# Kernel optimization log

Measured on AMD Instinct MI355X. Metric: run time of the kernel, lower is better.

Reference implementation:

```python
import jax, jax.numpy as jnp
import numpy as np

HIDDEN = 4544
N_HEADS = 71
HEAD_DIM = 64
SEQ = 2048
ROPE_BASE = 10000.0


def _rope_cos_sin(seq_len, dim, base=ROPE_BASE):
    inv_freq = 1.0 / (base ** (jnp.arange(0, dim, 2, dtype=jnp.float32) / dim))
    t = jnp.arange(seq_len, dtype=jnp.float32)
    freqs = jnp.einsum('i,j->ij', t, inv_freq)          # [s, dim/2]
    emb = jnp.concatenate([freqs, freqs], axis=-1)      # [s, dim]
    return jnp.cos(emb), jnp.sin(emb)


def _rotate_half(x):
    x1, x2 = jnp.split(x, 2, axis=-1)
    return jnp.concatenate([-x2, x1], axis=-1)


def _apply_rope(x, cos, sin):
    # x: [..., s, d]; cos/sin: [s, d] broadcast over leading dims
    return x * cos + _rotate_half(x) * sin


def setup_inputs() -> dict:
    key = jax.random.key(0)
    k1, k2, k3 = jax.random.split(key, 3)
    hidden_states = jax.random.normal(k1, (1, 1, SEQ, HIDDEN), dtype=jnp.float32) * 0.02
    qkv_weight = jax.random.normal(k2, ((N_HEADS + 2) * HEAD_DIM, HIDDEN), dtype=jnp.float32) * 0.02
    dense_weight = jax.random.normal(k3, (HIDDEN, HIDDEN), dtype=jnp.float32) * 0.02
    # causal additive mask, same construction as the torch module (triu of -1e5)
    mask = jnp.triu(jnp.full((SEQ, SEQ), -100000.0, dtype=jnp.float32), k=1)[None, None]
    return {
        'hidden_states': hidden_states,
        'qkv_weight': qkv_weight,
        'dense_weight': dense_weight,
        'attention_mask': mask,
    }


def reference(hidden_states, qkv_weight, dense_weight, attention_mask):
    b = hidden_states.shape[0]
    s = hidden_states.shape[2]
    x = hidden_states[:, 0]                                   # [b, s, H]

    # fused QKV projection (no bias): [b, s, (nH+2)*d]
    fused = jnp.einsum('bsh,oh->bso', x, qkv_weight)

    q = fused[..., : N_HEADS * HEAD_DIM]
    q = q.reshape(b, s, N_HEADS, HEAD_DIM).transpose(0, 2, 1, 3)   # [b, nH, s, d]
    k = fused[..., N_HEADS * HEAD_DIM : (N_HEADS + 1) * HEAD_DIM]  # [b, s, d] (single KV head, MQA)
    v = fused[..., (N_HEADS + 1) * HEAD_DIM :]                     # [b, s, d]

    cos, sin = _rope_cos_sin(s, HEAD_DIM)
    q = _apply_rope(q, cos, sin)
    k = _apply_rope(k, cos, sin)

    scale = 1.0 / np.sqrt(HEAD_DIM).astype(np.float32)
    scores = jnp.einsum('bhqd,bkd->bhqk', q, k) * scale            # [b, nH, s, s]
    scores = scores + attention_mask
    attn = jax.nn.softmax(scores, axis=-1)
    out = jnp.einsum('bhqk,bkd->bhqd', attn, v)                    # [b, nH, s, d]

    out = out.transpose(0, 2, 1, 3).reshape(b, s, N_HEADS * HEAD_DIM)  # concat heads
    out = jnp.einsum('bsh,oh->bso', out, dense_weight)             # dense projection
    return out[:, None]                                            # [b, 1, s, H]
```

## Files before the change

### kernel.cpp

```cpp
#include <hip/hip_runtime.h>

#define SEQ     2048
#define HIDDEN  4544
#define NHEAD   71
#define HD      64
#define QKV_OUT 4672

typedef __bf16    bf16;
typedef _Float16  f16;
typedef __bf16    bf16x8 __attribute__((ext_vector_type(8)));
typedef __bf16    bf16x4 __attribute__((ext_vector_type(4)));
typedef _Float16  f16x4  __attribute__((ext_vector_type(4)));
typedef _Float16  f16x8  __attribute__((ext_vector_type(8)));
typedef float     f32x4  __attribute__((ext_vector_type(4)));

__device__ inline void gl2lds16(const void* g, void* ldsbase) {
  __builtin_amdgcn_global_load_lds(
      (const __attribute__((address_space(1))) unsigned int*)g,
      (__attribute__((address_space(3))) unsigned int*)ldsbase,
      16, 0, 0);
}

__global__ void cvt3_k(const float* __restrict__ a, const float* __restrict__ b,
                       const float* __restrict__ c,
                       bf16* __restrict__ oa, bf16* __restrict__ ob, bf16* __restrict__ oc,
                       int na4, int nb4, int nc4) {
  int i = blockIdx.x * blockDim.x + threadIdx.x;
  const float* src; bf16* dst; int idx;
  if (i < na4)             { src = a; dst = oa; idx = i; }
  else if (i < na4 + nb4)  { src = b; dst = ob; idx = i - na4; }
  else if (i < na4 + nb4 + nc4) { src = c; dst = oc; idx = i - na4 - nb4; }
  else return;
  float4 f = ((const float4*)src)[idx];
  bf16x4 o;
  o[0] = (bf16)f.x; o[1] = (bf16)f.y; o[2] = (bf16)f.z; o[3] = (bf16)f.w;
  *(bf16x4*)(dst + (size_t)idx * 4) = o;
}

__global__ __launch_bounds__(256) void gemm_bt_k(const bf16* __restrict__ A,
                                                 const bf16* __restrict__ B,
                                                 float* __restrict__ C,
                                                 int K, int Nmat, int ldc) {
  __shared__ bf16 lA[2][128 * 32];
  __shared__ bf16 lB[2][128 * 32];
  const int t = threadIdx.x;
  const int lane = t & 63, w = t >> 6;

  const int gx = gridDim.x;
  const int nwg = gx * gridDim.y;
  const int orig = blockIdx.y * gx + blockIdx.x;
  const int swz = (orig & 7) * (nwg >> 3) + (orig >> 3);
  const int m0 = (swz % gx) * 128;
  const int n0 = (swz / gx) * 128;

  const int wm = (w >> 1) * 64, wn = (w & 1) * 64;
  const int qi = lane & 15, grp = lane >> 4;

  const int r0 = t >> 2;
  const int c0 = (t & 3) * 8;
  const bf16* gA0 = A + (size_t)(m0 + r0) * K + c0;
  const bf16* gA1 = A + (size_t)(m0 + 64 + r0) * K + c0;
  int bR0 = n0 + r0;      if (bR0 >= Nmat) bR0 = Nmat - 1;
  int bR1 = n0 + 64 + r0; if (bR1 >= Nmat) bR1 = Nmat - 1;
  const bf16* gB0 = B + (size_t)bR0 * K + c0;
  const bf16* gB1 = B + (size_t)bR1 * K + c0;
  bf16* lA00 = &lA[0][0] + w * 512;
  bf16* lA01 = &lA[0][2048] + w * 512;
  bf16* lA10 = &lA[1][0] + w * 512;
  bf16* lA11 = &lA[1][2048] + w * 512;
  bf16* lB00 = &lB[0][0] + w * 512;
  bf16* lB01 = &lB[0][2048] + w * 512;
  bf16* lB10 = &lB[1][0] + w * 512;
  bf16* lB11 = &lB[1][2048] + w * 512;

  f32x4 acc[4][4] = {};
  for (int k0 = 0; k0 < K; k0 += 64) {
    __syncthreads();
    gl2lds16(gA0 + k0,      lA00);
    gl2lds16(gA1 + k0,      lA01);
    gl2lds16(gA0 + k0 + 32, lA10);
    gl2lds16(gA1 + k0 + 32, lA11);
    gl2lds16(gB0 + k0,      lB00);
    gl2lds16(gB1 + k0,      lB01);
    gl2lds16(gB0 + k0 + 32, lB10);
    gl2lds16(gB1 + k0 + 32, lB11);
    __syncthreads();
#pragma unroll
    for (int half = 0; half < 2; ++half) {
      bf16x8 af[4], bfv[4];
#pragma unroll
      for (int i = 0; i < 4; ++i)
        af[i] = *(const bf16x8*)&lA[half][(wm + i * 16 + qi) * 32 + grp * 8];
#pragma unroll
      for (int i = 0; i < 4; ++i)
        bfv[i] = *(const bf16x8*)&lB[half][(wn + i * 16 + qi) * 32 + grp * 8];
#pragma unroll
      for (int i = 0; i < 4; ++i)
#pragma unroll
        for (int j = 0; j < 4; ++j)
          acc[i][j] = __builtin_amdgcn_mfma_f32_16x16x32_bf16(af[i], bfv[j], acc[i][j], 0, 0, 0);
    }
  }

#pragma unroll
  for (int i = 0; i < 4; ++i) {
    const int row = m0 + wm + i * 16 + grp * 4;
#pragma unroll
    for (int j = 0; j < 4; ++j) {
      const int col = n0 + wn + j * 16 + qi;
      if (col < Nmat) {
#pragma unroll
        for (int r = 0; r < 4; ++r)
          C[(size_t)(row + r) * ldc + col] = acc[i][j][r];
      }
    }
  }
}

#define QSCALE 0.18033688f
__global__ __launch_bounds__(256) void ropekv_k(const float* __restrict__ fused,
                                                bf16* __restrict__ Qb,
                                                bf16* __restrict__ Kf,
                                                f16* __restrict__ Vf) {
  const int s = blockIdx.x, t = threadIdx.x;
  __shared__ float cs[64], sn[64];
  if (t < 64) {
    int i = t & 31;
    double invf = pow(10000.0, -(double)i / 32.0);
    double ang = (double)s * invf;
    cs[t] = (float)cos(ang);
    sn[t] = (float)sin(ang);
  }
  __syncthreads();
  const float* row = fused + (size_t)s * QKV_OUT;

  if (t < 64) {
    const int d = t;
    float x = row[NHEAD * 64 + d], xp = row[NHEAD * 64 + (d ^ 32)];
    float rot = (d < 32) ? -xp : xp;
    Kf[(s >> 4) * 1024 + (d >> 5) * 512 + ((d >> 3) & 3) * 128 + (s & 15) * 8 + (d & 7)] =
        (bf16)(x * cs[d] + rot * sn[d]);
  } else if (t < 128) {
    const int d = t - 64;
    Vf[(s >> 4) * 1024 + (d >> 5) * 512 + ((s >> 2) & 3) * 128 + (d & 15) * 8 +
       ((d >> 4) & 1) * 4 + (s & 3)] = (f16)row[(NHEAD + 1) * 64 + d];
  }

  bf16* qrow = Qb + (size_t)s * HIDDEN;
  for (int u = t; u < NHEAD * 8; u += 256) {
    const int head = u >> 3, c4 = (u & 7) * 4;
    const int e = head * 64 + c4;
    float4 lo = *(const float4*)(row + e);
    float4 hi = *(const float4*)(row + e + 32);
    float xl[4] = {lo.x, lo.y, lo.z, lo.w};
    float xh[4] = {hi.x, hi.y, hi.z, hi.w};
    bf16x4 qlo, qhi;
#pragma unroll
    for (int j = 0; j < 4; ++j) {
      const float c = cs[c4 + j], n = sn[c4 + j];
      qlo[j] = (bf16)((xl[j] * c - xh[j] * n) * QSCALE);
      qhi[j] = (bf16)((xh[j] * c + xl[j] * n) * QSCALE);
    }
    *(bf16x4*)(qrow + e) = qlo;
    *(bf16x4*)(qrow + e + 32) = qhi;
  }
}

__global__ __launch_bounds__(64) void attn_k(const bf16* __restrict__ Qb,
                                             const bf16* __restrict__ Kf,
                                             const f16*  __restrict__ Vf,
                                             bf16* __restrict__ Ao) {
  __shared__ float fl[2 * 16 * 68];
  const int h = blockIdx.y;
  const int b32 = gridDim.x - 1 - blockIdx.x;
  const int lane = threadIdx.x;
  const int qi = lane & 15, grp = lane >> 4;
  const int q0 = b32 * 32;
  const int lastT = b32 >> 1;

  bf16x8 qf[2][2];
#pragma unroll
  for (int qq = 0; qq < 2; ++qq) {
    const bf16* qb = Qb + (size_t)(q0 + qq * 16 + qi) * HIDDEN + h * 64 + grp * 8;
    qf[qq][0] = *(const bf16x8*)qb;
    qf[qq][1] = *(const bf16x8*)(qb + 32);
  }

  f32x4 o[2][4] = {};
  float l[2] = {0.f, 0.f};

  for (int kb = 0; kb <= lastT; ++kb) {
    const bf16* kfp = Kf + (size_t)kb * 4096 + lane * 8;
    bf16x8 kf[4][2];
#pragma unroll
    for (int kk = 0; kk < 4; ++kk) {
      kf[kk][0] = *(const bf16x8*)(kfp + kk * 1024);
      kf[kk][1] = *(const bf16x8*)(kfp + kk * 1024 + 512);
    }
    f32x4 s4[2][4];
#pragma unroll
    for (int qq = 0; qq < 2; ++qq)
#pragma unroll
      for (int kk = 0; kk < 4; ++kk) {
        f32x4 z = {};
        s4[qq][kk] = __builtin_amdgcn_mfma_f32_16x16x32_bf16(kf[kk][0], qf[qq][0], z, 0, 0, 0);
        s4[qq][kk] = __builtin_amdgcn_mfma_f32_16x16x32_bf16(kf[kk][1], qf[qq][1], s4[qq][kk], 0, 0, 0);
      }
    const f16* vfp = Vf + (size_t)kb * 4096 + lane * 8;
    f16x4 vf[4][4];
#pragma unroll
    for (int kk = 0; kk < 4; ++kk)
#pragma unroll
      for (int p = 0; p < 2; ++p) {
        f16x8 v8 = *(const f16x8*)(vfp + kk * 1024 + p * 512);
#pragma unroll
        for (int j = 0; j < 4; ++j) {
          vf[kk][2 * p][j]     = v8[j];
          vf[kk][2 * p + 1][j] = v8[4 + j];
        }
      }

    if (kb == lastT) {
      const int dq = q0 - kb * 64 + qi;
#pragma unroll
      for (int qq = 0; qq < 2; ++qq)
#pragma unroll
        for (int kk = 0; kk < 4; ++kk)
#pragma unroll
          for (int r = 0; r < 4; ++r)
            if (kk * 16 + grp * 4 + r > dq + qq * 16) s4[qq][kk][r] = -1e30f;
    }
    f16x4 pf[2][4];
#pragma unroll
    for (int qq = 0; qq < 2; ++qq) {
      float ls = 0.f;
#pragma unroll
      for (int kk = 0; kk < 4; ++kk) {
        float p0 = exp2f(s4[qq][kk][0]), p1 = exp2f(s4[qq][kk][1]);
        float p2 = exp2f(s4[qq][kk][2]), p3 = exp2f(s4[qq][kk][3]);
        ls += (p0 + p1) + (p2 + p3);
        pf[qq][kk][0] = (f16)p0; pf[qq][kk][1] = (f16)p1;
        pf[qq][kk][2] = (f16)p2; pf[qq][kk][3] = (f16)p3;
      }
      l[qq] += ls;
    }
#pragma unroll
    for (int qq = 0; qq < 2; ++qq)
#pragma unroll
      for (int tt = 0; tt < 4; ++tt)
#pragma unroll
        for (int kk = 0; kk < 4; ++kk)
          o[qq][tt] = __builtin_amdgcn_mfma_f32_16x16x16f16(pf[qq][kk], vf[kk][tt], o[qq][tt], 0, 0, 0);
  }

#pragma unroll
  for (int qq = 0; qq < 2; ++qq) {
    float lq = l[qq];
    lq += __shfl_xor(lq, 16);
    lq += __shfl_xor(lq, 32);
    const float inv = 1.0f / lq;
    const float i0 = __shfl(inv, grp * 4 + 0);
    const float i1 = __shfl(inv, grp * 4 + 1);
    const float i2 = __shfl(inv, grp * 4 + 2);
    const float i3 = __shfl(inv, grp * 4 + 3);
    float* flq = fl + qq * 1088;
#pragma unroll
    for (int tt = 0; tt < 4; ++tt) {
      flq[(grp * 4 + 0) * 68 + tt * 16 + qi] = o[qq][tt][0] * i0;
      flq[(grp * 4 + 1) * 68 + tt * 16 + qi] = o[qq][tt][1] * i1;
      flq[(grp * 4 + 2) * 68 + tt * 16 + qi] = o[qq][tt][2] * i2;
      flq[(grp * 4 + 3) * 68 + tt * 16 + qi] = o[qq][tt][3] * i3;
    }
  }
  __syncthreads();
  const int row = lane >> 2, c0 = (lane & 3) * 16;
#pragma unroll
  for (int qq = 0; qq < 2; ++qq) {
    const float* flq = fl + qq * 1088;
    bf16x8 w0, w1;
#pragma unroll
    for (int j = 0; j < 8; ++j) {
      w0[j] = (bf16)flq[row * 68 + c0 + j];
      w1[j] = (bf16)flq[row * 68 + c0 + 8 + j];
    }
    bf16* ob = Ao + (size_t)(q0 + qq * 16 + row) * HIDDEN + h * 64 + c0;
    *(bf16x8*)ob = w0;
    *(bf16x8*)(ob + 8) = w1;
  }
}

extern "C" void kernel_launch(void* const* d_in, const int* in_sizes, int n_in,
                              void* d_out, int out_size, void* d_ws, size_t ws_size,
                              hipStream_t stream) {
  (void)in_sizes; (void)n_in; (void)out_size; (void)ws_size;
  const float* hs   = (const float*)d_in[0];
  const float* wqkv = (const float*)d_in[1];
  const float* wd   = (const float*)d_in[2];
  float* out = (float*)d_out;

  char* ws = (char*)d_ws;
  size_t off = 0;
  auto alloc = [&](size_t b) -> char* {
    char* p = ws + off;
    off += (b + 255) & ~(size_t)255;
    return p;
  };
  bf16* Xb     = (bf16*)alloc((size_t)SEQ * HIDDEN * 2);
  bf16* Wqb    = (bf16*)alloc((size_t)QKV_OUT * HIDDEN * 2);
  bf16* Wdb    = (bf16*)alloc((size_t)HIDDEN * HIDDEN * 2);
  float* fused = (float*)alloc((size_t)SEQ * QKV_OUT * 4);
  bf16* Qb     = (bf16*)alloc((size_t)SEQ * HIDDEN * 2);
  bf16* Kf     = (bf16*)alloc((size_t)(SEQ / 16) * 1024 * 2);
  f16*  Vf     = (f16*)alloc((size_t)(SEQ / 16) * 1024 * 2);
  bf16* Ao     = (bf16*)fused;

  const int na4 = SEQ * HIDDEN / 4;
  const int nb4 = QKV_OUT * HIDDEN / 4;
  const int nc4 = HIDDEN * HIDDEN / 4;
  cvt3_k<<<(na4 + nb4 + nc4 + 255) / 256, 256, 0, stream>>>(
      hs, wqkv, wd, Xb, Wqb, Wdb, na4, nb4, nc4);
  gemm_bt_k<<<dim3(SEQ / 128, (QKV_OUT + 127) / 128), 256, 0, stream>>>(
      Xb, Wqb, fused, HIDDEN, QKV_OUT, QKV_OUT);
  ropekv_k<<<SEQ, 256, 0, stream>>>(fused, Qb, Kf, Vf);
  attn_k<<<dim3(SEQ / 32, NHEAD), 64, 0, stream>>>(Qb, Kf, Vf, Ao);
  gemm_bt_k<<<dim3(SEQ / 128, (HIDDEN + 127) / 128), 256, 0, stream>>>(
      Ao, Wdb, out, HIDDEN, HIDDEN, HIDDEN);
}
```

Baseline: 567.5 us.

## Double-buffer GEMM LDS staging and switch attention softmax to natural exp

The bf16 GEMM now stages the next 64-wide K tile into a second LDS buffer while MFMAs run on the current one. This replaces the two barriers per iteration with one, so global-to-LDS loads can overlap with compute, at the cost of doubling LDS use per block (64 KB). Separately, the Q scale changes from log2(e)/sqrt(d) to 1/sqrt(d) and the softmax exponent changes from exp2f to __expf. That is mathematically equivalent only if the hidden running-max and rescale code uses the same base.

Measured after the change: 646.2 us. +13.9%, slower.

```diff
diff --git a/kernel.cpp b/kernel.cpp
--- a/kernel.cpp
+++ b/kernel.cpp
@@ -41,8 +41,8 @@
                                                  const bf16* __restrict__ B,
                                                  float* __restrict__ C,
                                                  int K, int Nmat, int ldc) {
-  __shared__ bf16 lA[2][128 * 32];
-  __shared__ bf16 lB[2][128 * 32];
+  __shared__ bf16 lA[2][8192];
+  __shared__ bf16 lB[2][8192];
   const int t = threadIdx.x;
   const int lane = t & 63, w = t >> 6;
 
@@ -64,42 +64,42 @@
   int bR1 = n0 + 64 + r0; if (bR1 >= Nmat) bR1 = Nmat - 1;
   const bf16* gB0 = B + (size_t)bR0 * K + c0;
   const bf16* gB1 = B + (size_t)bR1 * K + c0;
-  bf16* lA00 = &lA[0][0] + w * 512;
-  bf16* lA01 = &lA[0][2048] + w * 512;
-  bf16* lA10 = &lA[1][0] + w * 512;
-  bf16* lA11 = &lA[1][2048] + w * 512;
-  bf16* lB00 = &lB[0][0] + w * 512;
-  bf16* lB01 = &lB[0][2048] + w * 512;
-  bf16* lB10 = &lB[1][0] + w * 512;
-  bf16* lB11 = &lB[1][2048] + w * 512;
+
+  auto stage = [&](int buf, int k0) {
+    gl2lds16(gA0 + k0,      &lA[buf][0]    + w * 512);
+    gl2lds16(gA1 + k0,      &lA[buf][2048] + w * 512);
+    gl2lds16(gA0 + k0 + 32, &lA[buf][4096] + w * 512);
+    gl2lds16(gA1 + k0 + 32, &lA[buf][6144] + w * 512);
+    gl2lds16(gB0 + k0,      &lB[buf][0]    + w * 512);
+    gl2lds16(gB1 + k0,      &lB[buf][2048] + w * 512);
+    gl2lds16(gB0 + k0 + 32, &lB[buf][4096] + w * 512);
+    gl2lds16(gB1 + k0 + 32, &lB[buf][6144] + w * 512);
+  };
+
+  const int NK = K >> 6;
+  stage(0, 0);
+  __syncthreads();
 
   f32x4 acc[4][4] = {};
-  for (int k0 = 0; k0 < K; k0 += 64) {
-    __syncthreads();
-    gl2lds16(gA0 + k0,      lA00);
-    gl2lds16(gA1 + k0,      lA01);
-    gl2lds16(gA0 + k0 + 32, lA10);
-    gl2lds16(gA1 + k0 + 32, lA11);
-    gl2lds16(gB0 + k0,      lB00);
-    gl2lds16(gB1 + k0,      lB01);
-    gl2lds16(gB0 + k0 + 32, lB10);
-    gl2lds16(gB1 + k0 + 32, lB11);
-    __syncthreads();
+  for (int kt = 0; kt < NK; ++kt) {
+    const int cur = kt & 1;
+    if (kt + 1 < NK) stage(cur ^ 1, (kt + 1) << 6);
 #pragma unroll
     for (int half = 0; half < 2; ++half) {
       bf16x8 af[4], bfv[4];
 #pragma unroll
       for (int i = 0; i < 4; ++i)
-        af[i] = *(const bf16x8*)&lA[half][(wm + i * 16 + qi) * 32 + grp * 8];
+        af[i] = *(const bf16x8*)&lA[cur][half * 4096 + (wm + i * 16 + qi) * 32 + grp * 8];
 #pragma unroll
       for (int i = 0; i < 4; ++i)
-        bfv[i] = *(const bf16x8*)&lB[half][(wn + i * 16 + qi) * 32 + grp * 8];
+        bfv[i] = *(const bf16x8*)&lB[cur][half * 4096 + (wn + i * 16 + qi) * 32 + grp * 8];
 #pragma unroll
       for (int i = 0; i < 4; ++i)
 #pragma unroll
         for (int j = 0; j < 4; ++j)
           acc[i][j] = __builtin_amdgcn_mfma_f32_16x16x32_bf16(af[i], bfv[j], acc[i][j], 0, 0, 0);
     }
+    __syncthreads();
   }
 
 #pragma unroll
@@ -117,7 +117,7 @@
   }
 }
 
-#define QSCALE 0.18033688f
+#define QSCALE 0.125f
 __global__ __launch_bounds__(256) void ropekv_k(const float* __restrict__ fused,
                                                 bf16* __restrict__ Qb,
                                                 bf16* __restrict__ Kf,
@@ -236,8 +236,8 @@
       float ls = 0.f;
 #pragma unroll
       for (int kk = 0; kk < 4; ++kk) {
-        float p0 = exp2f(s4[qq][kk][0]), p1 = exp2f(s4[qq][kk][1]);
-        float p2 = exp2f(s4[qq][kk][2]), p3 = exp2f(s4[qq][kk][3]);
+        float p0 = __expf(s4[qq][kk][0]), p1 = __expf(s4[qq][kk][1]);
+        float p2 = __expf(s4[qq][kk][2]), p3 = __expf(s4[qq][kk][3]);
         ls += (p0 + p1) + (p2 + p3);
         pf[qq][kk][0] = (f16)p0; pf[qq][kk][1] = (f16)p1;
         pf[qq][kk][2] = (f16)p2; pf[qq][kk][3] = (f16)p3;
```

## Fuse RoPE, Q scaling and K/V relayout into QKV GEMM epilogue

Applied to the files above, without the earlier changes.

The QKV GEMM is templated so its epilogue applies rotary embeddings and Q scaling, then writes bf16 Q, swizzled bf16 K and f16 V directly. This removes the separate ropekv kernel and the fp32 fused intermediate that was written and read back. In exchange, the epilogue computes sin/cos per element in registers and issues narrower, scattered stores. The attention softmax also moves from exp2f with a log2e-folded scale to __expf with a plain 0.125 scale, which adds a multiply per exponent.

After: 612.0 us. 7.8% more time.

```diff
diff --git a/kernel.cpp b/kernel.cpp
--- a/kernel.cpp
+++ b/kernel.cpp
@@ -37,9 +37,13 @@
   *(bf16x4*)(dst + (size_t)idx * 4) = o;
 }
 
+template <bool ROPE>
 __global__ __launch_bounds__(256) void gemm_bt_k(const bf16* __restrict__ A,
                                                  const bf16* __restrict__ B,
                                                  float* __restrict__ C,
+                                                 bf16* __restrict__ Qb,
+                                                 bf16* __restrict__ Kf,
+                                                 f16* __restrict__ Vf,
                                                  int K, int Nmat, int ldc) {
   __shared__ bf16 lA[2][128 * 32];
   __shared__ bf16 lB[2][128 * 32];
@@ -102,67 +106,76 @@
     }
   }
 
-#pragma unroll
-  for (int i = 0; i < 4; ++i) {
-    const int row = m0 + wm + i * 16 + grp * 4;
-#pragma unroll
-    for (int j = 0; j < 4; ++j) {
-      const int col = n0 + wn + j * 16 + qi;
-      if (col < Nmat) {
-#pragma unroll
-        for (int r = 0; r < 4; ++r)
-          C[(size_t)(row + r) * ldc + col] = acc[i][j][r];
-      }
-    }
-  }
-}
-
-#define QSCALE 0.18033688f
-__global__ __launch_bounds__(256) void ropekv_k(const float* __restrict__ fused,
-                                                bf16* __restrict__ Qb,
-                                                bf16* __restrict__ Kf,
-                                                f16* __restrict__ Vf) {
-  const int s = blockIdx.x, t = threadIdx.x;
-  __shared__ float cs[64], sn[64];
-  if (t < 64) {
-    int i = t & 31;
-    double invf = pow(10000.0, -(double)i / 32.0);
-    double ang = (double)s * invf;
-    cs[t] = (float)cos(ang);
-    sn[t] = (float)sin(ang);
-  }
-  __syncthreads();
-  const float* row = fused + (size_t)s * QKV_OUT;
-
-  if (t < 64) {
-    const int d = t;
-    float x = row[NHEAD * 64 + d], xp = row[NHEAD * 64 + (d ^ 32)];
-    float rot = (d < 32) ? -xp : xp;
-    Kf[(s >> 4) * 1024 + (d >> 5) * 512 + ((d >> 3) & 3) * 128 + (s & 15) * 8 + (d & 7)] =
-        (bf16)(x * cs[d] + rot * sn[d]);
-  } else if (t < 128) {
-    const int d = t - 64;
-    Vf[(s >> 4) * 1024 + (d >> 5) * 512 + ((s >> 2) & 3) * 128 + (d & 15) * 8 +
-       ((d >> 4) & 1) * 4 + (s & 3)] = (f16)row[(NHEAD + 1) * 64 + d];
-  }
-
-  bf16* qrow = Qb + (size_t)s * HIDDEN;
-  for (int u = t; u < NHEAD * 8; u += 256) {
-    const int head = u >> 3, c4 = (u & 7) * 4;
-    const int e = head * 64 + c4;
-    float4 lo = *(const float4*)(row + e);
-    float4 hi = *(const float4*)(row + e + 32);
-    float xl[4] = {lo.x, lo.y, lo.z, lo.w};
-    float xh[4] = {hi.x, hi.y, hi.z, hi.w};
-    bf16x4 qlo, qhi;
-#pragma unroll
-    for (int j = 0; j < 4; ++j) {
-      const float c = cs[c4 + j], n = sn[c4 + j];
-      qlo[j] = (bf16)((xl[j] * c - xh[j] * n) * QSCALE);
-      qhi[j] = (bf16)((xh[j] * c + xl[j] * n) * QSCALE);
-    }
-    *(bf16x4*)(qrow + e) = qlo;
-    *(bf16x4*)(qrow + e + 32) = qhi;
+  if constexpr (ROPE) {
+    const int head = (n0 + wn) >> 6;
+    if (head < NHEAD) {
+      const float invf0 = powf(10000.0f, -(float)qi / 32.0f);
+      const float invf1 = powf(10000.0f, -(float)(qi + 16) / 32.0f);
+#pragma unroll
+      for (int i = 0; i < 4; ++i) {
+#pragma unroll
+        for (int r = 0; r < 4; ++r) {
+          const int s = m0 + wm + i * 16 + grp * 4 + r;
+          float s0c, c0v, s1c, c1v;
+          sincosf((float)s * invf0, &s0c, &c0v);
+          sincosf((float)s * invf1, &s1c, &c1v);
+          const float x0 = acc[i][0][r], x1 = acc[i][1][r];
+          const float x2 = acc[i][2][r], x3 = acc[i][3][r];
+          bf16* qb = Qb + (size_t)s * HIDDEN + head * 64 + qi;
+          qb[0]  = (bf16)((x0 * c0v - x2 * s0c) * 0.125f);
+          qb[16] = (bf16)((x1 * c1v - x3 * s1c) * 0.125f);
+          qb[32] = (bf16)((x2 * c0v + x0 * s0c) * 0.125f);
+          qb[48] = (bf16)((x3 * c1v + x1 * s1c) * 0.125f);
+        }
+      }
+    } else if (head == NHEAD) {
+      const float invf0 = powf(10000.0f, -(float)qi / 32.0f);
+      const float invf1 = powf(10000.0f, -(float)(qi + 16) / 32.0f);
+      const int g0 = qi >> 3, d7 = qi & 7;
+#pragma unroll
+      for (int i = 0; i < 4; ++i) {
+#pragma unroll
+        for (int r = 0; r < 4; ++r) {
+          const int s = m0 + wm + i * 16 + grp * 4 + r;
+          float s0c, c0v, s1c, c1v;
+          sincosf((float)s * invf0, &s0c, &c0v);
+          sincosf((float)s * invf1, &s1c, &c1v);
+          const float x0 = acc[i][0][r], x1 = acc[i][1][r];
+          const float x2 = acc[i][2][r], x3 = acc[i][3][r];
+          bf16* kb = Kf + (s >> 4) * 1024 + (s & 15) * 8;
+          kb[g0 * 128 + d7]             = (bf16)(x0 * c0v - x2 * s0c);
+          kb[(2 + g0) * 128 + d7]       = (bf16)(x1 * c1v - x3 * s1c);
+          kb[512 + g0 * 128 + d7]       = (bf16)(x2 * c0v + x0 * s0c);
+          kb[512 + (2 + g0) * 128 + d7] = (bf16)(x3 * c1v + x1 * s1c);
+        }
+      }
+    } else if (head == NHEAD + 1) {
+#pragma unroll
+      for (int i = 0; i < 4; ++i) {
+#pragma unroll
+        for (int r = 0; r < 4; ++r) {
+          const int s = m0 + wm + i * 16 + grp * 4 + r;
+          f16* vb = Vf + (s >> 4) * 1024 + grp * 128 + r;
+#pragma unroll
+          for (int j = 0; j < 4; ++j)
+            vb[(j >> 1) * 512 + qi * 8 + (j & 1) * 4] = (f16)acc[i][j][r];
+        }
+      }
+    }
+  } else {
+#pragma unroll
+    for (int i = 0; i < 4; ++i) {
+      const int row = m0 + wm + i * 16 + grp * 4;
+#pragma unroll
+      for (int j = 0; j < 4; ++j) {
+        const int col = n0 + wn + j * 16 + qi;
+        if (col < Nmat) {
+#pragma unroll
+          for (int r = 0; r < 4; ++r)
+            C[(size_t)(row + r) * ldc + col] = acc[i][j][r];
+        }
+      }
+    }
   }
 }
 
@@ -236,8 +249,8 @@
       float ls = 0.f;
 #pragma unroll
       for (int kk = 0; kk < 4; ++kk) {
-        float p0 = exp2f(s4[qq][kk][0]), p1 = exp2f(s4[qq][kk][1]);
-        float p2 = exp2f(s4[qq][kk][2]), p3 = exp2f(s4[qq][kk][3]);
+        float p0 = __expf(s4[qq][kk][0]), p1 = __expf(s4[qq][kk][1]);
+        float p2 = __expf(s4[qq][kk][2]), p3 = __expf(s4[qq][kk][3]);
         ls += (p0 + p1) + (p2 + p3);
         pf[qq][kk][0] = (f16)p0; pf[qq][kk][1] = (f16)p1;
         pf[qq][kk][2] = (f16)p2; pf[qq][kk][3] = (f16)p3;
@@ -308,21 +321,19 @@
   bf16* Xb     = (bf16*)alloc((size_t)SEQ * HIDDEN * 2);
   bf16* Wqb    = (bf16*)alloc((size_t)QKV_OUT * HIDDEN * 2);
   bf16* Wdb    = (bf16*)alloc((size_t)HIDDEN * HIDDEN * 2);
-  float* fused = (float*)alloc((size_t)SEQ * QKV_OUT * 4);
   bf16* Qb     = (bf16*)alloc((size_t)SEQ * HIDDEN * 2);
   bf16* Kf     = (bf16*)alloc((size_t)(SEQ / 16) * 1024 * 2);
   f16*  Vf     = (f16*)alloc((size_t)(SEQ / 16) * 1024 * 2);
-  bf16* Ao     = (bf16*)fused;
+  bf16* Ao     = (bf16*)alloc((size_t)SEQ * HIDDEN * 2);
 
   const int na4 = SEQ * HIDDEN / 4;
   const int nb4 = QKV_OUT * HIDDEN / 4;
   const int nc4 = HIDDEN * HIDDEN / 4;
   cvt3_k<<<(na4 + nb4 + nc4 + 255) / 256, 256, 0, stream>>>(
       hs, wqkv, wd, Xb, Wqb, Wdb, na4, nb4, nc4);
-  gemm_bt_k<<<dim3(SEQ / 128, (QKV_OUT + 127) / 128), 256, 0, stream>>>(
-      Xb, Wqb, fused, HIDDEN, QKV_OUT, QKV_OUT);
-  ropekv_k<<<SEQ, 256, 0, stream>>>(fused, Qb, Kf, Vf);
+  gemm_bt_k<true><<<dim3(SEQ / 128, (QKV_OUT + 127) / 128), 256, 0, stream>>>(
+      Xb, Wqb, nullptr, Qb, Kf, Vf, HIDDEN, QKV_OUT, 0);
   attn_k<<<dim3(SEQ / 32, NHEAD), 64, 0, stream>>>(Qb, Kf, Vf, Ao);
-  gemm_bt_k<<<dim3(SEQ / 128, (HIDDEN + 127) / 128), 256, 0, stream>>>(
-      Ao, Wdb, out, HIDDEN, HIDDEN, HIDDEN);
-}
+  gemm_bt_k<false><<<dim3(SEQ / 128, (HIDDEN + 127) / 128), 256, 0, stream>>>(
+      Ao, Wdb, out, nullptr, nullptr, nullptr, HIDDEN, HIDDEN, HIDDEN);
+}
```
